# Kernel tuning notes

Measured on AMD Instinct MI355X. Metric: run time of the kernel, lower is better.

Reference implementation:

```python
import jax, jax.numpy as jnp
import numpy as np

T, B, I, H = 2048, 2048, 1, 20


def setup_inputs() -> dict:
    key = jax.random.key(0)
    k0, k1, k2, k3, k4 = jax.random.split(key, 5)
    x = jax.random.normal(k0, (T, B, I), dtype=jnp.float32)
    # Concatenated gate weights in order [f, i, o, c]; equivalent to the
    # module's 8 separate nn.Linear layers (wf/uf, wi/ui, wo/uo, wc/uc).
    W = jax.random.normal(k1, (4 * H, I), dtype=jnp.float32) * 0.2
    U = jax.random.normal(k2, (4 * H, H), dtype=jnp.float32) * 0.2
    bw = jax.random.normal(k3, (4 * H,), dtype=jnp.float32) * 0.1  # Linear(w*) biases
    bu = jax.random.normal(k4, (4 * H,), dtype=jnp.float32) * 0.1  # Linear(u*) biases
    return {"x": x, "W": W, "U": U, "bw": bw, "bu": bu}


def reference(x, W, U, bw, bu):
    h_dim = U.shape[1]
    b = x.shape[1]
    # Precompute input projections for all timesteps: (T, B, 4H).
    # Original adds both Linear biases (bw from w*, bu from u*) plus zero b*.
    xz = jnp.einsum('tbi,gi->tbg', x, W) + bw + bu

    def step(carry, xz_t):
        h, c = carry
        z = xz_t + h @ U.T  # (B, 4H)
        f, i, o, g = jnp.split(z, 4, axis=-1)
        f = jax.nn.sigmoid(f)
        i = jax.nn.sigmoid(i)
        o = jax.nn.sigmoid(o)
        g = jnp.tanh(g)
        c = f * c + i * g
        h = o * jnp.tanh(c)
        return (h, c), h

    h0 = jnp.zeros((b, h_dim), dtype=x.dtype)
    c0 = jnp.zeros((b, h_dim), dtype=x.dtype)
    (h_last, c_last), h_seq = jax.lax.scan(step, (h0, c0), xz)
    return h_seq, h_last, c_last
```

## Files before the change

kernel.cpp:

```cpp
#include <hip/hip_runtime.h>
#include <cstddef>


constexpr int T = 2048;
constexpr int B = 2048;
constexpr int H = 20;
constexpr int BPW = 3;
constexpr int SLOTS = 4;
constexpr int CHUNK = 16;
constexpr int NCH = T / CHUNK;

typedef float f2 __attribute__((ext_vector_type(2)));

__device__ __forceinline__ float rcp_f(float v) { return __builtin_amdgcn_rcpf(v); }
__device__ __forceinline__ float ex2(float v)   { return __builtin_amdgcn_exp2f(v); }

__global__ __launch_bounds__(64, 1)
void lstm_wave4(const float* __restrict__ xg, const float* __restrict__ Wg,
                const float* __restrict__ Ug, const float* __restrict__ bwg,
                const float* __restrict__ bug, float* __restrict__ out) {
  __shared__ float h_lds[2][SLOTS][H];
  __shared__ float x_lds[2][SLOTS][CHUNK];

  const int tid = threadIdx.x;
  const int bl  = tid / H;
  const int j   = tid % H;
  const int bg0 = blockIdx.x * BPW + bl;
  const bool st = (bl < BPW) && (bg0 < B);
  const int bgi = (bg0 < B) ? bg0 : (B - 1);

  constexpr float K1 = 1.44269504f;

  f2 u01[H], u23[H], w01, w23, b01, b23;
#pragma unroll
  for (int k = 0; k < H; ++k) {
    u01[k].x = Ug[(0 * H + j) * H + k] * (-K1);
    u01[k].y = Ug[(1 * H + j) * H + k] * (-K1);
    u23[k].x = Ug[(2 * H + j) * H + k] * (-K1);
    u23[k].y = Ug[(3 * H + j) * H + k] * (2.0f * K1);
  }
  w01.x = Wg[0 * H + j] * (-K1);      w01.y = Wg[1 * H + j] * (-K1);
  w23.x = Wg[2 * H + j] * (-K1);      w23.y = Wg[3 * H + j] * (2.0f * K1);
  b01.x = (bwg[0 * H + j] + bug[0 * H + j]) * (-K1);
  b01.y = (bwg[1 * H + j] + bug[1 * H + j]) * (-K1);
  b23.x = (bwg[2 * H + j] + bug[2 * H + j]) * (-K1);
  b23.y = (bwg[3 * H + j] + bug[3 * H + j]) * (2.0f * K1);

  for (int q = tid; q < 2 * SLOTS * H;     q += 64) (&h_lds[0][0][0])[q] = 0.f;
  for (int q = tid; q < 2 * SLOTS * CHUNK; q += 64) (&x_lds[0][0][0])[q] = 0.f;
  __builtin_amdgcn_wave_barrier();

  if (j < CHUNK) x_lds[0][bl][j] = xg[(size_t)j * B + bgi];
  float xnext = (j < CHUNK) ? xg[(size_t)(CHUNK + j) * B + bgi] : 0.f;
  __builtin_amdgcn_wave_barrier();

  float c = 0.f, hn = 0.f;
  float xv = x_lds[0][bl][0];

  float* outp = out + (size_t)bgi * H + j;
  constexpr size_t OSTRIDE = (size_t)B * H;

  for (int ch = 0; ch < NCH; ++ch) {
    const int cb = ch & 1;
    if (j < CHUNK) {
      x_lds[cb ^ 1][bl][j] = xnext;
      const int tp = (ch + 2) * CHUNK + j;
      xnext = (tp < T) ? xg[(size_t)tp * B + bgi] : 0.f;
    }
#pragma unroll
    for (int s = 0; s < CHUNK; ++s) {
      const int p = s & 1;
      __builtin_amdgcn_wave_barrier();
      const float4* hp4 = reinterpret_cast<const float4*>(&h_lds[p][bl][0]);
      const float4 v0 = hp4[0], v1 = hp4[1], v2 = hp4[2], v3 = hp4[3], v4 = hp4[4];
      const float hb[H] = {v0.x, v0.y, v0.z, v0.w, v1.x, v1.y, v1.z, v1.w,
                           v2.x, v2.y, v2.z, v2.w, v3.x, v3.y, v3.z, v3.w,
                           v4.x, v4.y, v4.z, v4.w};
      const float xnv = (s + 1 < CHUNK) ? x_lds[cb][bl][s + 1]
                                        : x_lds[cb ^ 1][bl][0];
      f2 za01 = b01, za23 = b23;
      f2 zb01 = u01[10] * hb[10], zb23 = u23[10] * hb[10];
#pragma unroll
      for (int k = 0; k < 10; ++k) {
        za01 = u01[k] * hb[k] + za01;
        za23 = u23[k] * hb[k] + za23;
      }
#pragma unroll
      for (int k = 11; k < H; ++k) {
        zb01 = u01[k] * hb[k] + zb01;
        zb23 = u23[k] * hb[k] + zb23;
      }
      f2 xv2; xv2.x = xv; xv2.y = xv;
      const f2 z01 = w01 * xv2 + (za01 + zb01);
      const f2 z23 = w23 * xv2 + (za23 + zb23);
      const float fg = rcp_f(1.f + ex2(z01.x));
      const float ig = rcp_f(1.f + ex2(z01.y));
      const float og = rcp_f(1.f + ex2(z23.x));
      const float gt = fmaf(-2.f, rcp_f(1.f + ex2(z23.y)), 1.f);
      c = fmaf(fg, c, ig * gt);
      const float th = fmaf(-2.f, rcp_f(1.f + ex2(c * (2.f * K1))), 1.f);
      hn = og * th;
      h_lds[p ^ 1][bl][j] = hn;
      if (st) *outp = hn;
      outp += OSTRIDE;
      xv = xnv;
    }
  }
  if (st) {
    out[OSTRIDE * T + (size_t)bg0 * H + j] = hn;
    out[OSTRIDE * T + OSTRIDE + (size_t)bg0 * H + j] = c;
  }
}

extern "C" void kernel_launch(void* const* d_in, const int* in_sizes, int n_in,
                              void* d_out, int out_size, void* d_ws, size_t ws_size,
                              hipStream_t stream) {
  (void)in_sizes; (void)n_in; (void)d_ws; (void)ws_size; (void)out_size;
  const float* x  = (const float*)d_in[0];
  const float* W  = (const float*)d_in[1];
  const float* U  = (const float*)d_in[2];
  const float* bw = (const float*)d_in[3];
  const float* bu = (const float*)d_in[4];
  float* out = (float*)d_out;

  const int grid = (B + BPW - 1) / BPW;
  lstm_wave4<<<dim3(grid), dim3(64), 0, stream>>>(x, W, U, bw, bu, out);
}
```

Measured before the change: 482.8 us.

## Interleave two independent batch groups per wave to hide recurrence latency

Each 64-lane wave now carries two independent groups of three batch rows and alternates their timestep updates, so one group's LDS round trip and transcendental latency can overlap with the other group's math. The hidden-state read for the next step is moved to right after the write, into registers. This halves the grid size, leaving fewer waves to hide latency, and doubles the serial work per wave. It also adds register pressure from a second state set.

```diff
diff --git a/kernel.cpp b/kernel.cpp
--- a/kernel.cpp
+++ b/kernel.cpp
@@ -5,8 +5,10 @@
 constexpr int T = 2048;
 constexpr int B = 2048;
 constexpr int H = 20;
-constexpr int BPW = 3;
+constexpr int GR = 3;
 constexpr int SLOTS = 4;
+constexpr int D = 2;
+constexpr int BPW = GR * D;
 constexpr int CHUNK = 16;
 constexpr int NCH = T / CHUNK;
 
@@ -16,18 +18,21 @@
 __device__ __forceinline__ float ex2(float v)   { return __builtin_amdgcn_exp2f(v); }
 
 __global__ __launch_bounds__(64, 1)
-void lstm_wave4(const float* __restrict__ xg, const float* __restrict__ Wg,
+void lstm_wave5(const float* __restrict__ xg, const float* __restrict__ Wg,
                 const float* __restrict__ Ug, const float* __restrict__ bwg,
                 const float* __restrict__ bug, float* __restrict__ out) {
-  __shared__ float h_lds[2][SLOTS][H];
-  __shared__ float x_lds[2][SLOTS][CHUNK];
+  __shared__ float h_lds[D][2][SLOTS][H];
+  __shared__ float x_lds[D][2][SLOTS][CHUNK];
 
   const int tid = threadIdx.x;
   const int bl  = tid / H;
   const int j   = tid % H;
-  const int bg0 = blockIdx.x * BPW + bl;
-  const bool st = (bl < BPW) && (bg0 < B);
-  const int bgi = (bg0 < B) ? bg0 : (B - 1);
+  const int b0  = blockIdx.x * BPW;
+  const int bgA0 = b0 + bl, bgB0 = b0 + GR + bl;
+  const bool stA = (bl < GR) && (bgA0 < B);
+  const bool stB = (bl < GR) && (bgB0 < B);
+  const int bgiA = (bgA0 < B) ? bgA0 : (B - 1);
+  const int bgiB = (bgB0 < B) ? bgB0 : (B - 1);
 
   constexpr float K1 = 1.44269504f;
 
@@ -39,76 +44,105 @@
     u23[k].x = Ug[(2 * H + j) * H + k] * (-K1);
     u23[k].y = Ug[(3 * H + j) * H + k] * (2.0f * K1);
   }
-  w01.x = Wg[0 * H + j] * (-K1);      w01.y = Wg[1 * H + j] * (-K1);
-  w23.x = Wg[2 * H + j] * (-K1);      w23.y = Wg[3 * H + j] * (2.0f * K1);
+  w01.x = Wg[0 * H + j] * (-K1);   w01.y = Wg[1 * H + j] * (-K1);
+  w23.x = Wg[2 * H + j] * (-K1);   w23.y = Wg[3 * H + j] * (2.0f * K1);
   b01.x = (bwg[0 * H + j] + bug[0 * H + j]) * (-K1);
   b01.y = (bwg[1 * H + j] + bug[1 * H + j]) * (-K1);
   b23.x = (bwg[2 * H + j] + bug[2 * H + j]) * (-K1);
   b23.y = (bwg[3 * H + j] + bug[3 * H + j]) * (2.0f * K1);
 
-  for (int q = tid; q < 2 * SLOTS * H;     q += 64) (&h_lds[0][0][0])[q] = 0.f;
-  for (int q = tid; q < 2 * SLOTS * CHUNK; q += 64) (&x_lds[0][0][0])[q] = 0.f;
+  for (int q = tid; q < D * 2 * SLOTS * H;     q += 64) (&h_lds[0][0][0][0])[q] = 0.f;
+  for (int q = tid; q < D * 2 * SLOTS * CHUNK; q += 64) (&x_lds[0][0][0][0])[q] = 0.f;
   __builtin_amdgcn_wave_barrier();
 
-  if (j < CHUNK) x_lds[0][bl][j] = xg[(size_t)j * B + bgi];
-  float xnext = (j < CHUNK) ? xg[(size_t)(CHUNK + j) * B + bgi] : 0.f;
+  if (j < CHUNK) {
+    x_lds[0][0][bl][j] = xg[(size_t)j * B + bgiA];
+    x_lds[1][0][bl][j] = xg[(size_t)j * B + bgiB];
+  }
+  float xnA = (j < CHUNK) ? xg[(size_t)(CHUNK + j) * B + bgiA] : 0.f;
+  float xnB = (j < CHUNK) ? xg[(size_t)(CHUNK + j) * B + bgiB] : 0.f;
   __builtin_amdgcn_wave_barrier();
 
-  float c = 0.f, hn = 0.f;
-  float xv = x_lds[0][bl][0];
+  float4 hA4[5], hB4[5];
+#pragma unroll
+  for (int q = 0; q < 5; ++q) {
+    hA4[q] = make_float4(0.f, 0.f, 0.f, 0.f);
+    hB4[q] = make_float4(0.f, 0.f, 0.f, 0.f);
+  }
+  float cA = 0.f, cB = 0.f, hnA = 0.f, hnB = 0.f;
+  float xvA = x_lds[0][0][bl][0];
+  float xvB = x_lds[1][0][bl][0];
 
-  float* outp = out + (size_t)bgi * H + j;
-  constexpr size_t OSTRIDE = (size_t)B * H;
+  float* outA = out + (size_t)bgiA * H + j;
+  float* outB = out + (size_t)bgiB * H + j;
+  constexpr size_t OS = (size_t)B * H;
+
+#define SEG(REC, H4, CC, HNN, XV, OUTP, ST)                                    \
+  {                                                                            \
+    const float hb[H] = {H4[0].x, H4[0].y, H4[0].z, H4[0].w,                   \
+                         H4[1].x, H4[1].y, H4[1].z, H4[1].w,                   \
+                         H4[2].x, H4[2].y, H4[2].z, H4[2].w,                   \
+                         H4[3].x, H4[3].y, H4[3].z, H4[3].w,                   \
+                         H4[4].x, H4[4].y, H4[4].z, H4[4].w};                  \
+    const float xnv = (s + 1 < CHUNK) ? x_lds[REC][cb][bl][s + 1]              \
+                                      : x_lds[REC][cb ^ 1][bl][0];             \
+    f2 za01 = b01, za23 = b23;                                                 \
+    f2 zb01 = u01[10] * hb[10], zb23 = u23[10] * hb[10];                       \
+    _Pragma("unroll")                                                          \
+    for (int k = 0; k < 10; ++k) {                                             \
+      za01 = u01[k] * hb[k] + za01;                                            \
+      za23 = u23[k] * hb[k] + za23;                                            \
+    }                                                                          \
+    _Pragma("unroll")                                                          \
+    for (int k = 11; k < H; ++k) {                                             \
+      zb01 = u01[k] * hb[k] + zb01;                                            \
+      zb23 = u23[k] * hb[k] + zb23;                                            \
+    }                                                                          \
+    f2 xv2; xv2.x = (XV); xv2.y = (XV);                                        \
+    const f2 z01 = w01 * xv2 + (za01 + zb01);                                  \
+    const f2 z23 = w23 * xv2 + (za23 + zb23);                                  \
+    const float fg = rcp_f(1.f + ex2(z01.x));                                  \
+    const float ig = rcp_f(1.f + ex2(z01.y));                                  \
+    const float og = rcp_f(1.f + ex2(z23.x));                                  \
+    const float gt = fmaf(-2.f, rcp_f(1.f + ex2(z23.y)), 1.f);                 \
+    CC = fmaf(fg, CC, ig * gt);                                                \
+    const float th = fmaf(-2.f, rcp_f(1.f + ex2(CC * (2.f * K1))), 1.f);       \
+    HNN = og * th;                                                             \
+    h_lds[REC][pn][bl][j] = HNN;                                               \
+    asm volatile("" ::: "memory");        \
+    const float4* hp = reinterpret_cast<const float4*>(&h_lds[REC][pn][bl][0]);\
+    H4[0] = hp[0]; H4[1] = hp[1]; H4[2] = hp[2]; H4[3] = hp[3]; H4[4] = hp[4]; \
+    if (ST) *OUTP = HNN;                                                       \
+    OUTP += OS;                                                                \
+    XV = xnv;                                                                  \
+  }
 
   for (int ch = 0; ch < NCH; ++ch) {
     const int cb = ch & 1;
     if (j < CHUNK) {
-      x_lds[cb ^ 1][bl][j] = xnext;
+      x_lds[0][cb ^ 1][bl][j] = xnA;
+      x_lds[1][cb ^ 1][bl][j] = xnB;
       const int tp = (ch + 2) * CHUNK + j;
-      xnext = (tp < T) ? xg[(size_t)tp * B + bgi] : 0.f;
+      xnA = (tp < T) ? xg[(size_t)tp * B + bgiA] : 0.f;
+      xnB = (tp < T) ? xg[(size_t)tp * B + bgiB] : 0.f;
     }
 #pragma unroll
     for (int s = 0; s < CHUNK; ++s) {
-      const int p = s & 1;
+      const int pn = s & 1;
       __builtin_amdgcn_wave_barrier();
-      const float4* hp4 = reinterpret_cast<const float4*>(&h_lds[p][bl][0]);
-      const float4 v0 = hp4[0], v1 = hp4[1], v2 = hp4[2], v3 = hp4[3], v4 = hp4[4];
-      const float hb[H] = {v0.x, v0.y, v0.z, v0.w, v1.x, v1.y, v1.z, v1.w,
-                           v2.x, v2.y, v2.z, v2.w, v3.x, v3.y, v3.z, v3.w,
-                           v4.x, v4.y, v4.z, v4.w};
-      const float xnv = (s + 1 < CHUNK) ? x_lds[cb][bl][s + 1]
-                                        : x_lds[cb ^ 1][bl][0];
-      f2 za01 = b01, za23 = b23;
-      f2 zb01 = u01[10] * hb[10], zb23 = u23[10] * hb[10];
-#pragma unroll
-      for (int k = 0; k < 10; ++k) {
-        za01 = u01[k] * hb[k] + za01;
-        za23 = u23[k] * hb[k] + za23;
-      }
-#pragma unroll
-      for (int k = 11; k < H; ++k) {
-        zb01 = u01[k] * hb[k] + zb01;
-        zb23 = u23[k] * hb[k] + zb23;
-      }
-      f2 xv2; xv2.x = xv; xv2.y = xv;
-      const f2 z01 = w01 * xv2 + (za01 + zb01);
-      const f2 z23 = w23 * xv2 + (za23 + zb23);
-      const float fg = rcp_f(1.f + ex2(z01.x));
-      const float ig = rcp_f(1.f + ex2(z01.y));
-      const float og = rcp_f(1.f + ex2(z23.x));
-      const float gt = fmaf(-2.f, rcp_f(1.f + ex2(z23.y)), 1.f);
-      c = fmaf(fg, c, ig * gt);
-      const float th = fmaf(-2.f, rcp_f(1.f + ex2(c * (2.f * K1))), 1.f);
-      hn = og * th;
-      h_lds[p ^ 1][bl][j] = hn;
-      if (st) *outp = hn;
-      outp += OSTRIDE;
-      xv = xnv;
+      SEG(0, hA4, cA, hnA, xvA, outA, stA)
+      SEG(1, hB4, cB, hnB, xvB, outB, stB)
     }
   }
-  if (st) {
-    out[OSTRIDE * T + (size_t)bg0 * H + j] = hn;
-    out[OSTRIDE * T + OSTRIDE + (size_t)bg0 * H + j] = c;
+#undef SEG
+
+  if (stA) {
+    out[OS * T + (size_t)bgA0 * H + j] = hnA;
+    out[OS * (T + 1) + (size_t)bgA0 * H + j] = cA;
+  }
+  if (stB) {
+    out[OS * T + (size_t)bgB0 * H + j] = hnB;
+    out[OS * (T + 1) + (size_t)bgB0 * H + j] = cB;
   }
 }
 
@@ -124,5 +158,5 @@
   float* out = (float*)d_out;
 
   const int grid = (B + BPW - 1) / BPW;
-  lstm_wave4<<<dim3(grid), dim3(64), 0, stream>>>(x, W, U, bw, bu, out);
+  lstm_wave5<<<dim3(grid), dim3(64), 0, stream>>>(x, W, U, bw, bu, out);
 }
```

Result: slower. 899.4 us (+86.3%).

## Exchange hidden state via ds_bpermute instead of LDS round-trips

Applied to the files above, without the earlier changes.

Drops the shared-memory buffers for h and x. The hidden state is broadcast across lanes with ds_bpermute, one per k per step, and the x chunk is held in registers and fetched by permute. This removes the LDS store, wave barrier and reload on the serial recurrence path. The FMA chain is split into four accumulators for more ILP, and the cell state is kept pre-scaled by 2*log2(e) to save a multiply per step. The cost is 20 bpermute ops per step in place of 5 float4 LDS reads, which could add latency.

```diff
diff --git a/kernel.cpp b/kernel.cpp
--- a/kernel.cpp
+++ b/kernel.cpp
@@ -5,8 +5,7 @@
 constexpr int T = 2048;
 constexpr int B = 2048;
 constexpr int H = 20;
-constexpr int BPW = 3;
-constexpr int SLOTS = 4;
+constexpr int GR = 3;
 constexpr int CHUNK = 16;
 constexpr int NCH = T / CHUNK;
 
@@ -16,17 +15,14 @@
 __device__ __forceinline__ float ex2(float v)   { return __builtin_amdgcn_exp2f(v); }
 
 __global__ __launch_bounds__(64, 1)
-void lstm_wave4(const float* __restrict__ xg, const float* __restrict__ Wg,
+void lstm_bperm(const float* __restrict__ xg, const float* __restrict__ Wg,
                 const float* __restrict__ Ug, const float* __restrict__ bwg,
                 const float* __restrict__ bug, float* __restrict__ out) {
-  __shared__ float h_lds[2][SLOTS][H];
-  __shared__ float x_lds[2][SLOTS][CHUNK];
-
   const int tid = threadIdx.x;
   const int bl  = tid / H;
   const int j   = tid % H;
-  const int bg0 = blockIdx.x * BPW + bl;
-  const bool st = (bl < BPW) && (bg0 < B);
+  const int bg0 = blockIdx.x * GR + bl;
+  const bool st = (bl < GR) && (bg0 < B);
   const int bgi = (bg0 < B) ? bg0 : (B - 1);
 
   constexpr float K1 = 1.44269504f;
@@ -39,76 +35,74 @@
     u23[k].x = Ug[(2 * H + j) * H + k] * (-K1);
     u23[k].y = Ug[(3 * H + j) * H + k] * (2.0f * K1);
   }
-  w01.x = Wg[0 * H + j] * (-K1);      w01.y = Wg[1 * H + j] * (-K1);
-  w23.x = Wg[2 * H + j] * (-K1);      w23.y = Wg[3 * H + j] * (2.0f * K1);
+  w01.x = Wg[0 * H + j] * (-K1);   w01.y = Wg[1 * H + j] * (-K1);
+  w23.x = Wg[2 * H + j] * (-K1);   w23.y = Wg[3 * H + j] * (2.0f * K1);
   b01.x = (bwg[0 * H + j] + bug[0 * H + j]) * (-K1);
   b01.y = (bwg[1 * H + j] + bug[1 * H + j]) * (-K1);
   b23.x = (bwg[2 * H + j] + bug[2 * H + j]) * (-K1);
   b23.y = (bwg[3 * H + j] + bug[3 * H + j]) * (2.0f * K1);
 
-  for (int q = tid; q < 2 * SLOTS * H;     q += 64) (&h_lds[0][0][0])[q] = 0.f;
-  for (int q = tid; q < 2 * SLOTS * CHUNK; q += 64) (&x_lds[0][0][0])[q] = 0.f;
-  __builtin_amdgcn_wave_barrier();
+  const int pbase = bl * (H * 4);
 
-  if (j < CHUNK) x_lds[0][bl][j] = xg[(size_t)j * B + bgi];
-  float xnext = (j < CHUNK) ? xg[(size_t)(CHUNK + j) * B + bgi] : 0.f;
-  __builtin_amdgcn_wave_barrier();
+  const int jj = (j < CHUNK) ? j : (CHUNK - 1);
+  float xr = xg[(size_t)jj * B + bgi];
+  float xn = xg[(size_t)(CHUNK + jj) * B + bgi];
 
-  float c = 0.f, hn = 0.f;
-  float xv = x_lds[0][bl][0];
-
+  float c2 = 0.f;
+  float hn = 0.f;
   float* outp = out + (size_t)bgi * H + j;
-  constexpr size_t OSTRIDE = (size_t)B * H;
+  constexpr size_t OS = (size_t)B * H;
 
   for (int ch = 0; ch < NCH; ++ch) {
-    const int cb = ch & 1;
-    if (j < CHUNK) {
-      x_lds[cb ^ 1][bl][j] = xnext;
-      const int tp = (ch + 2) * CHUNK + j;
-      xnext = (tp < T) ? xg[(size_t)tp * B + bgi] : 0.f;
-    }
 #pragma unroll
     for (int s = 0; s < CHUNK; ++s) {
-      const int p = s & 1;
-      __builtin_amdgcn_wave_barrier();
-      const float4* hp4 = reinterpret_cast<const float4*>(&h_lds[p][bl][0]);
-      const float4 v0 = hp4[0], v1 = hp4[1], v2 = hp4[2], v3 = hp4[3], v4 = hp4[4];
-      const float hb[H] = {v0.x, v0.y, v0.z, v0.w, v1.x, v1.y, v1.z, v1.w,
-                           v2.x, v2.y, v2.z, v2.w, v3.x, v3.y, v3.z, v3.w,
-                           v4.x, v4.y, v4.z, v4.w};
-      const float xnv = (s + 1 < CHUNK) ? x_lds[cb][bl][s + 1]
-                                        : x_lds[cb ^ 1][bl][0];
-      f2 za01 = b01, za23 = b23;
-      f2 zb01 = u01[10] * hb[10], zb23 = u23[10] * hb[10];
+      const float xv = __int_as_float(
+          __builtin_amdgcn_ds_bpermute(pbase + 4 * s, __float_as_int(xr)));
+      const int hsrc = __float_as_int(hn);
+      f2 h2[H];
 #pragma unroll
-      for (int k = 0; k < 10; ++k) {
-        za01 = u01[k] * hb[k] + za01;
-        za23 = u23[k] * hb[k] + za23;
-      }
-#pragma unroll
-      for (int k = 11; k < H; ++k) {
-        zb01 = u01[k] * hb[k] + zb01;
-        zb23 = u23[k] * hb[k] + zb23;
+      for (int k = 0; k < H; ++k) {
+        const float hk = __int_as_float(
+            __builtin_amdgcn_ds_bpermute(pbase + 4 * k, hsrc));
+        h2[k].x = hk; h2[k].y = hk;
       }
       f2 xv2; xv2.x = xv; xv2.y = xv;
-      const f2 z01 = w01 * xv2 + (za01 + zb01);
-      const f2 z23 = w23 * xv2 + (za23 + zb23);
+      f2 qa01 = w01 * xv2 + b01,      qa23 = w23 * xv2 + b23;
+      f2 qb01 = u01[5]  * h2[5],      qb23 = u23[5]  * h2[5];
+      f2 qc01 = u01[10] * h2[10],     qc23 = u23[10] * h2[10];
+      f2 qd01 = u01[15] * h2[15],     qd23 = u23[15] * h2[15];
+#pragma unroll
+      for (int k = 0; k < 5; ++k)  { qa01 = u01[k] * h2[k] + qa01;
+                                     qa23 = u23[k] * h2[k] + qa23; }
+#pragma unroll
+      for (int k = 6; k < 10; ++k) { qb01 = u01[k] * h2[k] + qb01;
+                                     qb23 = u23[k] * h2[k] + qb23; }
+#pragma unroll
+      for (int k = 11; k < 15; ++k){ qc01 = u01[k] * h2[k] + qc01;
+                                     qc23 = u23[k] * h2[k] + qc23; }
+#pragma unroll
+      for (int k = 16; k < 20; ++k){ qd01 = u01[k] * h2[k] + qd01;
+                                     qd23 = u23[k] * h2[k] + qd23; }
+      const f2 z01 = (qa01 + qb01) + (qc01 + qd01);
+      const f2 z23 = (qa23 + qb23) + (qc23 + qd23);
       const float fg = rcp_f(1.f + ex2(z01.x));
       const float ig = rcp_f(1.f + ex2(z01.y));
       const float og = rcp_f(1.f + ex2(z23.x));
       const float gt = fmaf(-2.f, rcp_f(1.f + ex2(z23.y)), 1.f);
-      c = fmaf(fg, c, ig * gt);
-      const float th = fmaf(-2.f, rcp_f(1.f + ex2(c * (2.f * K1))), 1.f);
-      hn = og * th;
-      h_lds[p ^ 1][bl][j] = hn;
+      const float igt2 = (2.f * K1 * ig) * gt;
+      c2 = fmaf(fg, c2, igt2);
+      const float r = rcp_f(1.f + ex2(c2));
+      hn = fmaf(-2.f * og, r, og);
       if (st) *outp = hn;
-      outp += OSTRIDE;
-      xv = xnv;
+      outp += OS;
     }
+    xr = xn;
+    if (ch + 2 < NCH) xn = xg[(size_t)((ch + 2) * CHUNK + jj) * B + bgi];
   }
+
   if (st) {
-    out[OSTRIDE * T + (size_t)bg0 * H + j] = hn;
-    out[OSTRIDE * T + OSTRIDE + (size_t)bg0 * H + j] = c;
+    out[OS * T + (size_t)bg0 * H + j] = hn;
+    out[OS * (T + 1) + (size_t)bg0 * H + j] = c2 * 0.34657359f;
   }
 }
 
@@ -123,6 +117,6 @@
   const float* bu = (const float*)d_in[4];
   float* out = (float*)d_out;
 
-  const int grid = (B + BPW - 1) / BPW;
-  lstm_wave4<<<dim3(grid), dim3(64), 0, stream>>>(x, W, U, bw, bu, out);
+  const int grid = (B + GR - 1) / GR;
+  lstm_bperm<<<dim3(grid), dim3(64), 0, stream>>>(x, W, U, bw, bu, out);
 }
```

Result: slower. 624.2 us (+29.3%).
